# Performance work log

Hardware: AMD Instinct MI355X
Metric: run time of the kernel (lower is better)

The kernel has to match this reference:

```python
import jax, jax.numpy as jnp
import numpy as np

B, S, E, A = 4, 2048, 1024, 1024


def setup_inputs() -> dict:
    key = jax.random.key(0)
    k0, k1, k2, k3 = jax.random.split(key, 4)
    scale = 1.0 / np.sqrt(E)
    return {
        "embeds": jax.random.normal(k0, (B, S, E), dtype=jnp.float32),
        "Wq": jax.random.normal(k1, (E, A), dtype=jnp.float32) * scale,
        "Wk": jax.random.normal(k2, (E, A), dtype=jnp.float32) * scale,
        "Wv": jax.random.normal(k3, (E, A), dtype=jnp.float32) * scale,
    }


def reference(embeds, Wq, Wk, Wv):
    # projections: [B, S, A]
    q = jnp.einsum("bse,ea->bsa", embeds, Wq)
    k = jnp.einsum("bse,ea->bsa", embeds, Wk)
    v = jnp.einsum("bse,ea->bsa", embeds, Wv)
    attn_dim = k.shape[-1]
    # scores: [B, S, S], scaled by sqrt(attention_dim)
    scores = jnp.einsum("bqa,bka->bqk", q, k) / jnp.sqrt(
        jnp.asarray(attn_dim, dtype=q.dtype)
    )
    seq = scores.shape[-1]
    causal = jnp.tril(jnp.ones((seq, seq), dtype=bool))  # [S, S]
    scores = jnp.where(causal[None, :, :], scores, -jnp.inf)
    probs = jax.nn.softmax(scores, axis=-1)
    return jnp.einsum("bqk,bka->bqa", probs, v)
```

## Files before the change

### kernel.cpp

```cpp
#include <hip/hip_runtime.h>
#include <hip/hip_bf16.h>

#define DI __device__ __forceinline__

typedef __attribute__((ext_vector_type(8))) __bf16 bf16x8;
typedef __attribute__((ext_vector_type(4))) float f32x4;
typedef __attribute__((ext_vector_type(8))) short short8;
typedef __attribute__((ext_vector_type(4))) short short4v;
typedef unsigned short u16;

static constexpr int BB = 4, SS = 2048, EE = 1024, AA = 1024;

DI float bf2f(u16 u) { unsigned v = ((unsigned)u) << 16; float f; __builtin_memcpy(&f, &v, 4); return f; }
DI u16 f2bf(float f) { __hip_bfloat16 h = __float2bfloat16(f); u16 u; __builtin_memcpy(&u, &h, 2); return u; }

DI void gload16(const void* g, void* l) {
  __builtin_amdgcn_global_load_lds((const __attribute__((address_space(1))) void*)g,
                                   (__attribute__((address_space(3))) void*)l, 16, 0, 0);
}

DI int xcd_swz(int lin, int nwg) {
  int cpx = nwg >> 3;
  return (lin & 7) * cpx + (lin >> 3);
}

DI void stage_tile(const u16* g, int ld, char* lds, int wid, int lane) {
#pragma unroll
  for (int i = 0; i < 4; ++i) {
    int blk = i * 4 + wid;
    int r = blk * 8 + (lane >> 3);
    int c = (lane & 7) ^ (r & 7);
    gload16((const char*)(g + (size_t)r * ld) + c * 16, lds + blk * 1024);
  }
}

DI bf16x8 read_frag(const char* lds, int R, int c) {
  return *(const bf16x8*)(lds + R * 128 + ((c ^ (R & 7)) << 4));
}

DI void gemm_tile(const u16* Ap, int lda, const u16* Bp, int ldb, int ksteps,
                  char* As, char* Bs, f32x4 acc[4][4]) {
  const int tid = threadIdx.x, lane = tid & 63, wid = tid >> 6;
  const int wr = wid >> 1, wc = wid & 1;
  for (int ks = 0; ks < ksteps; ++ks) {
    __syncthreads();
    stage_tile(Ap + (size_t)ks * 64, lda, As, wid, lane);
    stage_tile(Bp + (size_t)ks * 64, ldb, Bs, wid, lane);
    asm volatile("s_waitcnt vmcnt(0)" ::: "memory");
    __syncthreads();
#pragma unroll
    for (int ksub = 0; ksub < 2; ++ksub) {
      const int c = ksub * 4 + (lane >> 4);
      bf16x8 af[4], bfr[4];
#pragma unroll
      for (int mi = 0; mi < 4; ++mi) af[mi] = read_frag(As, wr * 64 + mi * 16 + (lane & 15), c);
#pragma unroll
      for (int ni = 0; ni < 4; ++ni) bfr[ni] = read_frag(Bs, wc * 64 + ni * 16 + (lane & 15), c);
#pragma unroll
      for (int mi = 0; mi < 4; ++mi)
#pragma unroll
        for (int ni = 0; ni < 4; ++ni)
          acc[mi][ni] = __builtin_amdgcn_mfma_f32_16x16x32_bf16(af[mi], bfr[ni], acc[mi][ni], 0, 0, 0);
    }
  }
}

DI void store_tile_bf16(u16* Op, int ldc, float scale, f32x4 acc[4][4], int r0, int c0, int lane) {
#pragma unroll
  for (int mi = 0; mi < 4; ++mi)
#pragma unroll
    for (int ni = 0; ni < 4; ++ni)
#pragma unroll
      for (int r = 0; r < 4; ++r) {
        int row = r0 + mi * 16 + ((lane >> 4) << 2) + r;
        int col = c0 + ni * 16 + (lane & 15);
        Op[(size_t)row * ldc + col] = f2bf(acc[mi][ni][r] * scale);
      }
}

__global__ __launch_bounds__(256) void k_castx(const float* __restrict__ X, u16* __restrict__ Xb) {
  size_t i = ((size_t)blockIdx.x * 256 + threadIdx.x) * 4;
  f32x4 f = *(const f32x4*)(X + i);
  short4v o;
#pragma unroll
  for (int j = 0; j < 4; ++j) o[j] = (short)f2bf(f[j]);
  *(short4v*)(Xb + i) = o;
}

__global__ __launch_bounds__(256) void k_wt(const float* __restrict__ Wq, const float* __restrict__ Wk,
                                            const float* __restrict__ Wv, u16* __restrict__ Wt) {
  __shared__ float t[64][65];
  const int k0 = blockIdx.x * 64, n0 = blockIdx.y * 64, w = blockIdx.z;
  const float* W = (w == 0) ? Wq : ((w == 1) ? Wk : Wv);
  u16* Wo = Wt + (size_t)w * EE * AA;
  const int tx = threadIdx.x & 63, ty = threadIdx.x >> 6;
#pragma unroll
  for (int r = 0; r < 16; ++r) {
    int k = r * 4 + ty;
    t[k][tx] = W[(size_t)(k0 + k) * AA + n0 + tx];
  }
  __syncthreads();
#pragma unroll
  for (int r = 0; r < 16; ++r) {
    int n = r * 4 + ty;
    Wo[(size_t)(n0 + n) * EE + k0 + tx] = f2bf(t[tx][n]);
  }
}

__global__ __launch_bounds__(256) void k_proj(const u16* __restrict__ Xb, const u16* __restrict__ Wt,
                                              u16* __restrict__ Out) {
  __shared__ __align__(16) char smem[32768];
  const int lin = blockIdx.y * gridDim.x + blockIdx.x;
  const int wg = xcd_swz(lin, 512);
  const int nt = wg & 7, mt = wg >> 3, w = blockIdx.z;
  const u16* Ap = Xb + (size_t)mt * 128 * EE;
  const u16* Bp = Wt + (size_t)w * EE * AA + (size_t)nt * 128 * EE;
  u16* Op = Out + (size_t)w * (size_t)(BB * SS) * AA;
  f32x4 acc[4][4];
#pragma unroll
  for (int i = 0; i < 4; ++i)
#pragma unroll
    for (int j = 0; j < 4; ++j) acc[i][j] = (f32x4)0.f;
  gemm_tile(Ap, EE, Bp, EE, EE / 64, smem, smem + 16384, acc);
  const int lane = threadIdx.x & 63, wid = threadIdx.x >> 6;
  store_tile_bf16(Op, AA, 1.f, acc, mt * 128 + (wid >> 1) * 64, nt * 128 + (wid & 1) * 64, lane);
}

__global__ __launch_bounds__(256) void k_vt(const u16* __restrict__ V, u16* __restrict__ Vt) {
  __shared__ u16 t[64][66];
  const int s0 = blockIdx.x * 64, a0 = blockIdx.y * 64, b = blockIdx.z;
  const u16* Vb = V + (size_t)b * SS * AA;
  u16* Vo = Vt + (size_t)b * AA * SS;
  const int tx = threadIdx.x & 63, ty = threadIdx.x >> 6;
#pragma unroll
  for (int r = 0; r < 16; ++r) {
    int s = r * 4 + ty;
    t[s][tx] = Vb[(size_t)(s0 + s) * AA + a0 + tx];
  }
  __syncthreads();
#pragma unroll
  for (int r = 0; r < 16; ++r) {
    int a = r * 4 + ty;
    Vo[(size_t)(a0 + a) * SS + s0 + tx] = t[tx][a];
  }
}

__global__ __launch_bounds__(256) void k_scores(const u16* __restrict__ Q, const u16* __restrict__ K,
                                                u16* __restrict__ Sc, float* __restrict__ rowsum) {
  __shared__ __align__(16) char smem[32768];
  const int wg = xcd_swz(blockIdx.x, 544);
  const int b = wg / 136, t = wg % 136;
  int i = (int)((sqrtf(8.f * t + 1.f) - 1.f) * 0.5f);
  while ((i + 1) * (i + 2) / 2 <= t) ++i;
  while (i * (i + 1) / 2 > t) --i;
  const int j = t - i * (i + 1) / 2;
  const u16* Ap = Q + (size_t)b * SS * AA + (size_t)i * 128 * AA;
  const u16* Bp = K + (size_t)b * SS * AA + (size_t)j * 128 * AA;
  u16* Op = Sc + (size_t)b * SS * SS;
  float* rs = rowsum + (size_t)b * SS;
  f32x4 acc[4][4];
#pragma unroll
  for (int x = 0; x < 4; ++x)
#pragma unroll
    for (int y = 0; y < 4; ++y) acc[x][y] = (f32x4)0.f;
  gemm_tile(Ap, AA, Bp, AA, AA / 64, smem, smem + 16384, acc);
  const int lane = threadIdx.x & 63, wid = threadIdx.x >> 6;
  const int r0 = i * 128 + (wid >> 1) * 64, c0 = j * 128 + (wid & 1) * 64;
#pragma unroll
  for (int mi = 0; mi < 4; ++mi)
#pragma unroll
    for (int r = 0; r < 4; ++r) {
      const int row = r0 + mi * 16 + ((lane >> 4) << 2) + r;
      float psum = 0.f;
#pragma unroll
      for (int ni = 0; ni < 4; ++ni) {
        const int col = c0 + ni * 16 + (lane & 15);
        float e = (col <= row) ? __expf(acc[mi][ni][r] * 0.03125f) : 0.f;
        psum += e;
        Op[(size_t)row * SS + col] = f2bf(e);
      }
      psum += __shfl_xor(psum, 1, 16);
      psum += __shfl_xor(psum, 2, 16);
      psum += __shfl_xor(psum, 4, 16);
      psum += __shfl_xor(psum, 8, 16);
      if ((lane & 15) == 0) atomicAdd(&rs[row], psum);
    }
}

__global__ __launch_bounds__(256) void k_pv(const u16* __restrict__ Sc, const u16* __restrict__ Vt,
                                            const float* __restrict__ rowsum, float* __restrict__ Out) {
  __shared__ __align__(16) char smem[32768];
  const int lin = blockIdx.y * gridDim.x + blockIdx.x;
  const int wg = xcd_swz(lin, 512);
  const int nt = wg & 7, rest = wg >> 3;
  const int i = rest & 15, b = rest >> 4;
  const u16* Ap = Sc + (size_t)b * SS * SS + (size_t)i * 128 * SS;
  const u16* Bp = Vt + (size_t)b * AA * SS + (size_t)nt * 128 * SS;
  const float* rs = rowsum + (size_t)b * SS;
  float* Op = Out + (size_t)b * SS * AA;
  f32x4 acc[4][4];
#pragma unroll
  for (int x = 0; x < 4; ++x)
#pragma unroll
    for (int y = 0; y < 4; ++y) acc[x][y] = (f32x4)0.f;
  gemm_tile(Ap, SS, Bp, SS, 2 * (i + 1), smem, smem + 16384, acc);
  const int lane = threadIdx.x & 63, wid = threadIdx.x >> 6;
  const int r0 = i * 128 + (wid >> 1) * 64, c0 = nt * 128 + (wid & 1) * 64;
#pragma unroll
  for (int mi = 0; mi < 4; ++mi)
#pragma unroll
    for (int r = 0; r < 4; ++r) {
      const int row = r0 + mi * 16 + ((lane >> 4) << 2) + r;
      const float inv = 1.f / rs[row];
#pragma unroll
      for (int ni = 0; ni < 4; ++ni) {
        const int col = c0 + ni * 16 + (lane & 15);
        Op[(size_t)row * AA + col] = acc[mi][ni][r] * inv;
      }
    }
}

extern "C" void kernel_launch(void* const* d_in, const int* in_sizes, int n_in,
                              void* d_out, int out_size, void* d_ws, size_t ws_size,
                              hipStream_t stream) {
  const float* X  = (const float*)d_in[0];
  const float* Wq = (const float*)d_in[1];
  const float* Wk = (const float*)d_in[2];
  const float* Wv = (const float*)d_in[3];
  float* Out = (float*)d_out;
  char* ws = (char*)d_ws;
  u16* Xb = (u16*)ws;
  u16* Wt = (u16*)(ws + (16u << 20));
  u16* Qb = (u16*)(ws + (22u << 20));
  u16* Kb = (u16*)(ws + (38u << 20));
  u16* Vb = (u16*)(ws + (54u << 20));
  u16* Vt = (u16*)(ws + (70u << 20));
  u16* Sc = (u16*)(ws + (86u << 20));
  float* rowsum = (float*)(ws + (118u << 20));

  k_castx<<<dim3((BB * SS * EE) / (256 * 4)), 256, 0, stream>>>(X, Xb);
  k_wt<<<dim3(16, 16, 3), 256, 0, stream>>>(Wq, Wk, Wv, Wt);
  k_proj<<<dim3(AA / 128, (BB * SS) / 128, 3), 256, 0, stream>>>(Xb, Wt, Qb);
  k_vt<<<dim3(SS / 64, AA / 64, BB), 256, 0, stream>>>(Vb, Vt);
  hipMemsetAsync(rowsum, 0, BB * SS * sizeof(float), stream);
  k_scores<<<dim3(136 * BB), 256, 0, stream>>>(Qb, Kb, Sc, rowsum);
  k_pv<<<dim3(AA / 128, 16 * BB), 256, 0, stream>>>(Sc, Vt, rowsum, Out);
}
```

Measured before the change: 170.3 us.

## Replace projection GEMM with double-buffered 256x256 tile kernel; remap PV grid

Replaces the 128x128 projection GEMM with a 512-thread kernel computing 256x256 tiles over a fused Q/K/V weight matrix. It double-buffers LDS with async global-to-LDS loads and partial vmcnt waits so loads overlap MFMA work, and raises MFMA priority with setprio. The PV kernel's block-to-tile mapping is changed so each XCD works on the same query block (b,i) across nt tiles, aiming at better L2 reuse of score rows. The cost is 128KB of LDS per block and higher register pressure, which limits occupancy.

Result: slower. 174.7 us (+2.6%).

```diff
diff --git a/kernel.cpp b/kernel.cpp
--- a/kernel.cpp
+++ b/kernel.cpp
@@ -24,6 +24,102 @@
   return (lin & 7) * cpx + (lin >> 3);
 }
 
+DI bf16x8 read_frag(const char* lds, int R, int c) {
+  return *(const bf16x8*)(lds + R * 128 + ((c ^ (R & 7)) << 4));
+}
+
+static constexpr int PNK = EE / 64;
+
+__global__ __launch_bounds__(512, 2) void k_proj2(const u16* __restrict__ Xb, const u16* __restrict__ Wt,
+                                                  u16* __restrict__ Qb) {
+  __shared__ __align__(16) char smem[131072];
+  const int tid = threadIdx.x, lane = tid & 63, wid = tid >> 6;
+  const int wr = wid >> 2, wc = wid & 3;
+  const int lin = blockIdx.y * gridDim.x + blockIdx.x;
+  const int wg = xcd_swz(lin, 384);
+  const int mt = wg / 12, nt = wg % 12;
+  const u16* Ap = Xb + (size_t)mt * 256 * EE;
+  const u16* Bp = Wt + (size_t)nt * 256 * EE;
+
+  f32x4 acc[8][4];
+#pragma unroll
+  for (int i = 0; i < 8; ++i)
+#pragma unroll
+    for (int j = 0; j < 4; ++j) acc[i][j] = (f32x4)0.f;
+
+  auto STAGE = [&](int kt) {
+    char* As = smem + (kt & 1) * 65536;
+    char* Bs = As + 32768;
+    const u16* a = Ap + kt * 64;
+    const u16* b = Bp + kt * 64;
+#pragma unroll
+    for (int i = 0; i < 4; ++i) {
+      int blk = i * 8 + wid;
+      int r = blk * 8 + (lane >> 3);
+      int c = (lane & 7) ^ (r & 7);
+      gload16((const char*)(a + (size_t)r * EE) + c * 16, As + blk * 1024);
+      gload16((const char*)(b + (size_t)r * EE) + c * 16, Bs + blk * 1024);
+    }
+  };
+
+  STAGE(0);
+  STAGE(1);
+  for (int kt = 0; kt < PNK; ++kt) {
+    const char* As = smem + (kt & 1) * 65536;
+    const char* Bs = As + 32768;
+    if (kt + 1 < PNK) asm volatile("s_waitcnt vmcnt(8)" ::: "memory");
+    else              asm volatile("s_waitcnt vmcnt(0)" ::: "memory");
+    __builtin_amdgcn_sched_barrier(0);
+    __builtin_amdgcn_s_barrier();
+    __builtin_amdgcn_sched_barrier(0);
+    bf16x8 bfr[4][2];
+#pragma unroll
+    for (int ni = 0; ni < 4; ++ni)
+#pragma unroll
+      for (int ks = 0; ks < 2; ++ks)
+        bfr[ni][ks] = read_frag(Bs, wc * 64 + ni * 16 + (lane & 15), ks * 4 + (lane >> 4));
+#pragma unroll
+    for (int q = 0; q < 4; ++q) {
+      bf16x8 af[2][2];
+#pragma unroll
+      for (int m2 = 0; m2 < 2; ++m2)
+#pragma unroll
+        for (int ks = 0; ks < 2; ++ks)
+          af[m2][ks] = read_frag(As, wr * 128 + (q * 2 + m2) * 16 + (lane & 15), ks * 4 + (lane >> 4));
+      __builtin_amdgcn_s_setprio(1);
+#pragma unroll
+      for (int m2 = 0; m2 < 2; ++m2)
+#pragma unroll
+        for (int ni = 0; ni < 4; ++ni)
+#pragma unroll
+          for (int ks = 0; ks < 2; ++ks)
+            acc[q * 2 + m2][ni] =
+                __builtin_amdgcn_mfma_f32_16x16x32_bf16(af[m2][ks], bfr[ni][ks], acc[q * 2 + m2][ni], 0, 0, 0);
+      __builtin_amdgcn_s_setprio(0);
+    }
+    __builtin_amdgcn_sched_barrier(0);
+    __builtin_amdgcn_s_barrier();
+    __builtin_amdgcn_sched_barrier(0);
+    if (kt + 2 < PNK) STAGE(kt + 2);
+  }
+
+  const int lane15 = lane & 15, lhi = lane >> 4;
+  const int w = nt >> 2;
+  const int cb = (nt & 3) * 256 + wc * 64;
+  const int r0 = mt * 256 + wr * 128;
+  u16* Op = Qb + (size_t)w * ((size_t)BB * SS * AA);
+#pragma unroll
+  for (int mi = 0; mi < 8; ++mi)
+#pragma unroll
+    for (int ni = 0; ni < 4; ++ni)
+#pragma unroll
+      for (int r = 0; r < 4; ++r) {
+        int row = r0 + mi * 16 + lhi * 4 + r;
+        int col = cb + ni * 16 + lane15;
+        Op[(size_t)row * AA + col] = f2bf(acc[mi][ni][r]);
+      }
+}
+
 DI void stage_tile(const u16* g, int ld, char* lds, int wid, int lane) {
 #pragma unroll
   for (int i = 0; i < 4; ++i) {
@@ -32,10 +128,6 @@
     int c = (lane & 7) ^ (r & 7);
     gload16((const char*)(g + (size_t)r * ld) + c * 16, lds + blk * 1024);
   }
-}
-
-DI bf16x8 read_frag(const char* lds, int R, int c) {
-  return *(const bf16x8*)(lds + R * 128 + ((c ^ (R & 7)) << 4));
 }
 
 DI void gemm_tile(const u16* Ap, int lda, const u16* Bp, int ldb, int ksteps,
@@ -65,19 +157,6 @@
   }
 }
 
-DI void store_tile_bf16(u16* Op, int ldc, float scale, f32x4 acc[4][4], int r0, int c0, int lane) {
-#pragma unroll
-  for (int mi = 0; mi < 4; ++mi)
-#pragma unroll
-    for (int ni = 0; ni < 4; ++ni)
-#pragma unroll
-      for (int r = 0; r < 4; ++r) {
-        int row = r0 + mi * 16 + ((lane >> 4) << 2) + r;
-        int col = c0 + ni * 16 + (lane & 15);
-        Op[(size_t)row * ldc + col] = f2bf(acc[mi][ni][r] * scale);
-      }
-}
-
 __global__ __launch_bounds__(256) void k_castx(const float* __restrict__ X, u16* __restrict__ Xb) {
   size_t i = ((size_t)blockIdx.x * 256 + threadIdx.x) * 4;
   f32x4 f = *(const f32x4*)(X + i);
@@ -105,25 +184,6 @@
     int n = r * 4 + ty;
     Wo[(size_t)(n0 + n) * EE + k0 + tx] = f2bf(t[tx][n]);
   }
-}
-
-__global__ __launch_bounds__(256) void k_proj(const u16* __restrict__ Xb, const u16* __restrict__ Wt,
-                                              u16* __restrict__ Out) {
-  __shared__ __align__(16) char smem[32768];
-  const int lin = blockIdx.y * gridDim.x + blockIdx.x;
-  const int wg = xcd_swz(lin, 512);
-  const int nt = wg & 7, mt = wg >> 3, w = blockIdx.z;
-  const u16* Ap = Xb + (size_t)mt * 128 * EE;
-  const u16* Bp = Wt + (size_t)w * EE * AA + (size_t)nt * 128 * EE;
-  u16* Op = Out + (size_t)w * (size_t)(BB * SS) * AA;
-  f32x4 acc[4][4];
-#pragma unroll
-  for (int i = 0; i < 4; ++i)
-#pragma unroll
-    for (int j = 0; j < 4; ++j) acc[i][j] = (f32x4)0.f;
-  gemm_tile(Ap, EE, Bp, EE, EE / 64, smem, smem + 16384, acc);
-  const int lane = threadIdx.x & 63, wid = threadIdx.x >> 6;
-  store_tile_bf16(Op, AA, 1.f, acc, mt * 128 + (wid >> 1) * 64, nt * 128 + (wid & 1) * 64, lane);
 }
 
 __global__ __launch_bounds__(256) void k_vt(const u16* __restrict__ V, u16* __restrict__ Vt) {
@@ -191,18 +251,19 @@
                                             const float* __restrict__ rowsum, float* __restrict__ Out) {
   __shared__ __align__(16) char smem[32768];
   const int lin = blockIdx.y * gridDim.x + blockIdx.x;
-  const int wg = xcd_swz(lin, 512);
-  const int nt = wg & 7, rest = wg >> 3;
-  const int i = rest & 15, b = rest >> 4;
+  const int x = lin & 7, j = lin >> 3;
+  const int pair = x + 8 * (j >> 3);
+  const int nt = j & 7;
+  const int b = pair >> 4, i = pair & 15;
   const u16* Ap = Sc + (size_t)b * SS * SS + (size_t)i * 128 * SS;
   const u16* Bp = Vt + (size_t)b * AA * SS + (size_t)nt * 128 * SS;
   const float* rs = rowsum + (size_t)b * SS;
   float* Op = Out + (size_t)b * SS * AA;
   f32x4 acc[4][4];
 #pragma unroll
-  for (int x = 0; x < 4; ++x)
-#pragma unroll
-    for (int y = 0; y < 4; ++y) acc[x][y] = (f32x4)0.f;
+  for (int p = 0; p < 4; ++p)
+#pragma unroll
+    for (int q = 0; q < 4; ++q) acc[p][q] = (f32x4)0.f;
   gemm_tile(Ap, SS, Bp, SS, 2 * (i + 1), smem, smem + 16384, acc);
   const int lane = threadIdx.x & 63, wid = threadIdx.x >> 6;
   const int r0 = i * 128 + (wid >> 1) * 64, c0 = nt * 128 + (wid & 1) * 64;
@@ -240,9 +301,9 @@
 
   k_castx<<<dim3((BB * SS * EE) / (256 * 4)), 256, 0, stream>>>(X, Xb);
   k_wt<<<dim3(16, 16, 3), 256, 0, stream>>>(Wq, Wk, Wv, Wt);
-  k_proj<<<dim3(AA / 128, (BB * SS) / 128, 3), 256, 0, stream>>>(Xb, Wt, Qb);
+  k_proj2<<<dim3(12, 32), 512, 0, stream>>>(Xb, Wt, Qb);
   k_vt<<<dim3(SS / 64, AA / 64, BB), 256, 0, stream>>>(Vb, Vt);
   hipMemsetAsync(rowsum, 0, BB * SS * sizeof(float), stream);
   k_scores<<<dim3(136 * BB), 256, 0, stream>>>(Qb, Kb, Sc, rowsum);
-  k_pv<<<dim3(AA / 128, 16 * BB), 256, 0, stream>>>(Sc, Vt, rowsum, Out);
-}
+  k_pv<<<dim3(8, 64), 256, 0, stream>>>(Sc, Vt, rowsum, Out);
+}
```
